# Kernel optimization log

Hardware: AMD Instinct MI355X
Metric: run time of the kernel (lower is better)

## Reference

```python
import jax, jax.numpy as jnp
import numpy as np

EMBED_DIM = 1024
Q_HEADS = 16
KV_HEADS = 8            # n_heads // 2 per CrossAttention
HEAD_DIM = EMBED_DIM // Q_HEADS   # 64
KV_EMBED = HEAD_DIM * KV_HEADS    # 512
GROUPS = Q_HEADS // KV_HEADS      # 2
LN_EPS = 1e-5
RMS_EPS = 1e-6


def _rms_norm(x):
    # SimpleRMSNorm (no learned scale) used inside BitLinear
    return x * jax.lax.rsqrt(jnp.mean(jnp.square(x), axis=-1, keepdims=True) + RMS_EPS)


def _act_quant(x):
    # per-token 8-bit absmax activation quant (BitNet b1.58)
    scale = 127.0 / jnp.maximum(jnp.max(jnp.abs(x), axis=-1, keepdims=True), 1e-5)
    return jnp.clip(jnp.round(x * scale), -128.0, 127.0) / scale


def _weight_quant(w):
    # ternary {-1,0,1} absmean weight quant
    scale = 1.0 / jnp.maximum(jnp.mean(jnp.abs(w)), 1e-5)
    return jnp.clip(jnp.round(w * scale), -1.0, 1.0) / scale


def _ste(a, q):
    # straight-through estimator: forward=q, backward=identity
    return a + jax.lax.stop_gradient(q - a)


def bit_linear(x, w):
    # x: [b, n, in], w: [out, in] (torch Linear layout), no bias
    xn = _rms_norm(x)
    xq = _ste(xn, _act_quant(xn))
    wq = _ste(w, _weight_quant(w))
    return jnp.einsum('bni,oi->bno', xq, wq)


def setup_inputs() -> dict:
    key = jax.random.key(0)
    ks = jax.random.split(key, 6)
    B, N, S, D = 16, 1024, 256, EMBED_DIM
    s = D ** -0.5
    return {
        'x': jax.random.normal(ks[0], (B, N, D), jnp.float32),
        'y': jax.random.normal(ks[1], (B, S, D), jnp.float32),
        'wq': jax.random.normal(ks[2], (D, D), jnp.float32) * s,
        'wk': jax.random.normal(ks[3], (KV_EMBED, D), jnp.float32) * s,
        'wv': jax.random.normal(ks[4], (KV_EMBED, D), jnp.float32) * s,
        'wo': jax.random.normal(ks[5], (D, D), jnp.float32) * s,
        'ln_gamma': jnp.ones((D,), jnp.float32),
        'ln_beta': jnp.zeros((D,), jnp.float32),
    }


def reference(x, y, wq, wk, wv, wo, ln_gamma, ln_beta):
    B, N, D = x.shape
    S = y.shape[1]
    # ternary-quantized projections
    q = bit_linear(x, wq).reshape(B, N, Q_HEADS, HEAD_DIM)
    k = bit_linear(y, wk).reshape(B, S, KV_HEADS, HEAD_DIM)
    v = bit_linear(y, wv).reshape(B, S, KV_HEADS, HEAD_DIM)
    # grouped-query attention: split q heads as (kv_head, group)
    q = jnp.transpose(q, (0, 2, 1, 3)) / (HEAD_DIM ** 0.5)   # [b, Hq, n, d]
    q = q.reshape(B, KV_HEADS, GROUPS, N, HEAD_DIM)           # [b, h, g, n, d]
    k = jnp.transpose(k, (0, 2, 1, 3))                        # [b, h, s, d]
    v = jnp.transpose(v, (0, 2, 1, 3))
    scores = jnp.einsum('bhgnd,bhsd->bhgns', q, k)
    attn = jax.nn.softmax(scores, axis=-1)                    # is_causal=False, no mask
    out = jnp.einsum('bhgns,bhsd->bhgnd', attn, v)
    out = jnp.transpose(out, (0, 3, 1, 2, 4)).reshape(B, N, D)  # b n (h g) d -> b n D
    # LayerNorm before out projection
    mu = jnp.mean(out, axis=-1, keepdims=True)
    var = jnp.mean(jnp.square(out - mu), axis=-1, keepdims=True)
    out = (out - mu) * jax.lax.rsqrt(var + LN_EPS) * ln_gamma + ln_beta
    return bit_linear(out, wo)
```

## Files before the change

kernel.cpp:

```cpp
#include <hip/hip_runtime.h>
#include <hip/hip_bf16.h>

typedef int int4v __attribute__((ext_vector_type(4)));
typedef float float4v __attribute__((ext_vector_type(4)));
typedef _Float16 half8 __attribute__((ext_vector_type(8)));

#define DEV __device__ __forceinline__

DEV signed char quant8(float v) {
    int q = (int)rintf(v);
    q = q < -128 ? -128 : (q > 127 ? 127 : q);
    return (signed char)q;
}

DEV int tern1(float v) {
    int q = (int)rintf(v);
    q = q < -1 ? -1 : (q > 1 ? 1 : q);
    return q;
}

DEV void gl2lds16(const void* g, void* l) {
    __builtin_amdgcn_global_load_lds(
        (const __attribute__((address_space(1))) void*)g,
        (__attribute__((address_space(3))) void*)l, 16, 0, 0);
}

__global__ __launch_bounds__(256) void absmean_all(
    const float* __restrict__ WQ, const float* __restrict__ WK,
    const float* __restrict__ WV, const float* __restrict__ WO,
    double* __restrict__ part)
{
    __shared__ double red[256];
    int bx = blockIdx.x, t = threadIdx.x;
    const float* W; int rel;
    if (bx < 64)       { W = WQ; rel = bx; }
    else if (bx < 96)  { W = WK; rel = bx - 64; }
    else if (bx < 128) { W = WV; rel = bx - 96; }
    else               { W = WO; rel = bx - 128; }
    size_t base = (size_t)rel * 16384;
    double acc = 0.0;
    for (int i = t; i < 16384; i += 256) acc += (double)fabsf(W[base + i]);
    red[t] = acc; __syncthreads();
    #pragma unroll
    for (int o = 128; o > 0; o >>= 1) {
        if (t < o) red[t] += red[t + o];
        __syncthreads();
    }
    if (t == 0) part[bx] = red[0];
}

__global__ __launch_bounds__(256) void betas_kernel(
    const double* __restrict__ part, float* __restrict__ betas)
{
    int t = threadIdx.x, w = t >> 6, lane = t & 63;
    const int offs[4]   = {0, 64, 96, 128};
    const int cnts[4]   = {64, 32, 32, 64};
    const int counts[4] = {1048576, 524288, 524288, 1048576};
    double v = (lane < cnts[w]) ? part[offs[w] + lane] : 0.0;
    #pragma unroll
    for (int o = 32; o > 0; o >>= 1) v += __shfl_down(v, o);
    if (lane == 0) betas[w] = fmaxf((float)(v / (double)counts[w]), 1e-5f);
}

__global__ __launch_bounds__(256) void wquant_all(
    const float* __restrict__ WQ, const float* __restrict__ WK,
    const float* __restrict__ WV, const float* __restrict__ WO,
    signed char* __restrict__ w8, const float* __restrict__ betas)
{
    int bx = blockIdx.x;
    const float* W; signed char* O; float inv; int rel;
    if (bx < 1024)      { W = WQ; O = w8;                           rel = bx;        inv = 1.f / betas[0]; }
    else if (bx < 1536) { W = WK; O = w8 + (1 << 20);               rel = bx - 1024; inv = 1.f / betas[1]; }
    else if (bx < 2048) { W = WV; O = w8 + (1 << 20) + (512 << 10); rel = bx - 1536; inv = 1.f / betas[2]; }
    else                { W = WO; O = w8 + (2 << 20);               rel = bx - 2048; inv = 1.f / betas[3]; }
    int i = rel * 256 + threadIdx.x;
    float4 u = ((const float4*)W)[i];
    int q0 = tern1(u.x * inv);
    int q1 = tern1(u.y * inv);
    int q2 = tern1(u.z * inv);
    int q3 = tern1(u.w * inv);
    int packed = (q0 & 0xff) | ((q1 & 0xff) << 8) | ((q2 & 0xff) << 16) | ((q3 & 0xff) << 24);
    ((int*)O)[i] = packed;
}

__global__ __launch_bounds__(256) void act_quant(
    const float* __restrict__ X, signed char* __restrict__ X8,
    float* __restrict__ RS)
{
    int row = blockIdx.x * 4 + (threadIdx.x >> 6);
    int lane = threadIdx.x & 63;
    const float4* xr = (const float4*)(X + (size_t)row * 1024) + lane * 4;
    float4 u[4];
    #pragma unroll
    for (int i = 0; i < 4; i++) u[i] = xr[i];
    float ss = 0.f, am = 0.f;
    #pragma unroll
    for (int i = 0; i < 4; i++) {
        ss += u[i].x * u[i].x + u[i].y * u[i].y + u[i].z * u[i].z + u[i].w * u[i].w;
        am = fmaxf(am, fmaxf(fmaxf(fabsf(u[i].x), fabsf(u[i].y)),
                             fmaxf(fabsf(u[i].z), fabsf(u[i].w))));
    }
    #pragma unroll
    for (int o = 32; o > 0; o >>= 1) {
        ss += __shfl_xor(ss, o);
        am = fmaxf(am, __shfl_xor(am, o));
    }
    float r = 1.f / sqrtf(ss * (1.f / 1024.f) + 1e-6f);
    float m = fmaxf(am * r, 1e-5f);
    float s = 127.f / m;
    int pk[4];
    #pragma unroll
    for (int i = 0; i < 4; i++) {
        int q0 = quant8((u[i].x * r) * s);
        int q1 = quant8((u[i].y * r) * s);
        int q2 = quant8((u[i].z * r) * s);
        int q3 = quant8((u[i].w * r) * s);
        pk[i] = (q0 & 0xff) | ((q1 & 0xff) << 8) | ((q2 & 0xff) << 16) | ((q3 & 0xff) << 24);
    }
    int4v pv = {pk[0], pk[1], pk[2], pk[3]};
    ((int4v*)(X8 + (size_t)row * 1024))[lane] = pv;
    if (lane == 0) RS[row] = m * (1.f / 127.f);
}

__global__ __launch_bounds__(256) void gemm_i8(
    const signed char* __restrict__ A, const signed char* __restrict__ B,
    float* __restrict__ outF, _Float16* __restrict__ outH,
    _Float16* __restrict__ outK, _Float16* __restrict__ outV,
    int N, int K,
    const float* __restrict__ rowscale, const float* __restrict__ betas,
    int b0i, int b1i, int split, float extra, int mode)
{
    __shared__ __align__(16) signed char As[128 * 64];
    __shared__ __align__(16) signed char Bs[128 * 64];
    const int tid = threadIdx.x;
    const int lane = tid & 63, wid = tid >> 6;
    const int wr = wid >> 1, wc = wid & 1;
    const int lr = lane & 15, quad = lane >> 4;
    const int bM = blockIdx.y, bN = blockIdx.x;

    int4v zero = {0, 0, 0, 0};
    int4v acc[4][4];
    #pragma unroll
    for (int i = 0; i < 4; i++)
        #pragma unroll
        for (int j = 0; j < 4; j++) acc[i][j] = zero;

    const int srow = wid * 32 + (lane >> 2);
    const int soff = (lane & 3) * 16;
    const signed char* gA0 = A + (size_t)(bM * 128 + srow) * K + soff;
    const signed char* gA1 = gA0 + (size_t)16 * K;
    const signed char* gB0 = B + (size_t)(bN * 128 + srow) * K + soff;
    const signed char* gB1 = gB0 + (size_t)16 * K;
    signed char* lA0 = As + wid * 2048;
    signed char* lA1 = lA0 + 1024;
    signed char* lB0 = Bs + wid * 2048;
    signed char* lB1 = lB0 + 1024;

    for (int kb = 0; kb < K; kb += 64) {
        __syncthreads();
        gl2lds16(gA0 + kb, lA0);
        gl2lds16(gA1 + kb, lA1);
        gl2lds16(gB0 + kb, lB0);
        gl2lds16(gB1 + kb, lB1);
        __syncthreads();
        int4v af[4], bfr[4];
        #pragma unroll
        for (int tm = 0; tm < 4; tm++)
            af[tm] = *(const int4v*)(As + (wr * 64 + tm * 16 + lr) * 64 + quad * 16);
        #pragma unroll
        for (int tn = 0; tn < 4; tn++)
            bfr[tn] = *(const int4v*)(Bs + (wc * 64 + tn * 16 + lr) * 64 + quad * 16);
        #pragma unroll
        for (int tm = 0; tm < 4; tm++)
            #pragma unroll
            for (int tn = 0; tn < 4; tn++)
                acc[tm][tn] = __builtin_amdgcn_mfma_i32_16x16x64_i8(af[tm], bfr[tn], acc[tm][tn], 0, 0, 0);
    }

    const float s0 = betas[b0i] * extra, s1 = betas[b1i] * extra;
    #pragma unroll
    for (int tm = 0; tm < 4; tm++) {
        #pragma unroll
        for (int r = 0; r < 4; r++) {
            int grow = bM * 128 + wr * 64 + tm * 16 + quad * 4 + r;
            float rs = rowscale[grow];
            #pragma unroll
            for (int tn = 0; tn < 4; tn++) {
                int col = bN * 128 + wc * 64 + tn * 16 + lr;
                float v = (float)acc[tm][tn][r] * rs * (col < split ? s0 : s1);
                if (mode == 0) {
                    outF[(size_t)grow * N + col] = v;
                } else if (mode == 1) {
                    outH[(size_t)grow * 1024 + col] = (_Float16)v;
                } else {
                    if (col < 512)
                        outK[(size_t)grow * 512 + col] = (_Float16)v;
                    else
                        outV[((size_t)(grow >> 8) * 512 + (col - 512)) * 256 + (grow & 255)] = (_Float16)v;
                }
            }
        }
    }
}

__global__ __launch_bounds__(256, 4) void attn_mfma(
    const _Float16* Qh, const _Float16* __restrict__ Kh,
    const _Float16* __restrict__ Vt, _Float16* Oh)
{
    __shared__ __align__(16) _Float16 KVs[256 * 64];

    const int tid = threadIdx.x;
    const int lane = tid & 63;
    const int w = tid >> 6;
    const int lq = lane & 15;
    const int quad = lane >> 4;
    const int swz = (lq & 7) << 4;

    const int bx = blockIdx.x;
    const int nt = bx & 15, g = (bx >> 4) & 1, h = (bx >> 5) & 7, b = bx >> 8;
    const int rbase = b * 1024 + nt * 64 + w * 16;
    const int qcol0 = (h * 2 + g) * 64;

    half8 aq[2];
    #pragma unroll
    for (int ks = 0; ks < 2; ks++)
        aq[ks] = *(const half8*)(Qh + (size_t)(rbase + lq) * 1024 + qcol0 + ks * 32 + quad * 8);

    {
        int kb = tid >> 3;
        int c  = tid & 7;
        int rp = (kb & 3) | ((kb >> 1) & 12) | ((kb & 4) << 2);
        const _Float16* kg = Kh + (size_t)(b * 256 + kb) * 512 + h * 64 + c * 8;
        char* lb = (char*)KVs;
        #pragma unroll
        for (int j = 0; j < 8; j++) {
            int row = 32 * j + rp;
            int off = (row * 128 + c * 16) ^ ((row & 7) << 4);
            *(half8*)(lb + off) = *(const half8*)(kg + (size_t)32 * j * 512);
        }
    }
    __syncthreads();

    float4v acc[16];
    float4v zf = {0.f, 0.f, 0.f, 0.f};
    #pragma unroll
    for (int t = 0; t < 16; t++) acc[t] = zf;
    const int kc0 = (quad * 16) ^ swz;
    const int kc1 = (64 + quad * 16) ^ swz;
    #pragma unroll
    for (int t = 0; t < 16; t++) {
        const char* krow = (const char*)KVs + (t * 16 + lq) * 128;
        half8 kf0 = *(const half8*)(krow + kc0);
        acc[t] = __builtin_amdgcn_mfma_f32_16x16x32_f16(kf0, aq[0], acc[t], 0, 0, 0);
        half8 kf1 = *(const half8*)(krow + kc1);
        acc[t] = __builtin_amdgcn_mfma_f32_16x16x32_f16(kf1, aq[1], acc[t], 0, 0, 0);
    }

    float m = acc[0][0];
    #pragma unroll
    for (int t = 0; t < 16; t++) {
        #pragma unroll
        for (int r = 0; r < 4; r++) m = fmaxf(m, acc[t][r]);
    }
    m = fmaxf(m, __shfl_xor(m, 16));
    m = fmaxf(m, __shfl_xor(m, 32));
    float l = 0.f;
    #pragma unroll
    for (int t = 0; t < 16; t++) {
        #pragma unroll
        for (int r = 0; r < 4; r++) {
            float p = __expf(acc[t][r] - m);
            acc[t][r] = p;
            l += p;
        }
    }
    l += __shfl_xor(l, 16);
    l += __shfl_xor(l, 32);

    __syncthreads();

    {
        int row = tid >> 5, c = tid & 31;
        const _Float16* vg = Vt + ((size_t)b * 512 + h * 64 + row) * 256 + c * 8;
        char* lb = (char*)KVs;
        #pragma unroll
        for (int j = 0; j < 8; j++) {
            int rr = row + 8 * j;
            int off = (rr * 512 + c * 16) ^ ((rr & 7) << 4);
            *(half8*)(lb + off) = *(const half8*)(vg + (size_t)8 * j * 256);
        }
    }
    __syncthreads();

    float4v oacc[4];
    #pragma unroll
    for (int dt = 0; dt < 4; dt++) oacc[dt] = zf;
    #pragma unroll
    for (int ks = 0; ks < 8; ks++) {
        half8 pf;
        #pragma unroll
        for (int r = 0; r < 4; r++) {
            pf[r]     = (_Float16)acc[2 * ks][r];
            pf[4 + r] = (_Float16)acc[2 * ks + 1][r];
        }
        const int vc = (ks * 64 + quad * 16) ^ swz;
        #pragma unroll
        for (int dt = 0; dt < 4; dt++) {
            half8 bv = *(const half8*)((const char*)KVs + (dt * 16 + lq) * 512 + vc);
            oacc[dt] = __builtin_amdgcn_mfma_f32_16x16x32_f16(pf, bv, oacc[dt], 0, 0, 0);
        }
    }

    float linv = 1.f / l;
    float invr[4];
    #pragma unroll
    for (int r = 0; r < 4; r++) invr[r] = __shfl(linv, quad * 4 + r);
    #pragma unroll
    for (int dt = 0; dt < 4; dt++) {
        #pragma unroll
        for (int r = 0; r < 4; r++) {
            Oh[(size_t)(rbase + quad * 4 + r) * 1024 + qcol0 + dt * 16 + lq] =
                (_Float16)(oacc[dt][r] * invr[r]);
        }
    }
}

__global__ __launch_bounds__(256) void ln_quant(
    const _Float16* __restrict__ AO, const float* __restrict__ G,
    const float* __restrict__ Bt, signed char* __restrict__ O8,
    float* __restrict__ OS)
{
    int row = blockIdx.x * 4 + (threadIdx.x >> 6);
    int lane = threadIdx.x & 63;
    const _Float16* xr = AO + (size_t)row * 1024 + lane * 16;
    half8 h0 = *(const half8*)xr;
    half8 h1 = *(const half8*)(xr + 8);
    float x[16];
    #pragma unroll
    for (int i = 0; i < 8; i++) { x[i] = (float)h0[i]; x[8 + i] = (float)h1[i]; }
    float sx = 0.f, sx2 = 0.f;
    #pragma unroll
    for (int i = 0; i < 16; i++) { sx += x[i]; sx2 += x[i] * x[i]; }
    #pragma unroll
    for (int o = 32; o > 0; o >>= 1) {
        sx += __shfl_xor(sx, o);
        sx2 += __shfl_xor(sx2, o);
    }
    float mu = sx * (1.f / 1024.f);
    float var = sx2 * (1.f / 1024.f) - mu * mu;
    float rstd = 1.f / sqrtf(var + 1e-5f);

    const float4* gp = (const float4*)(G + lane * 16);
    const float4* bp = (const float4*)(Bt + lane * 16);
    float l[16];
    #pragma unroll
    for (int i = 0; i < 4; i++) {
        float4 gv = gp[i], bv = bp[i];
        l[i * 4 + 0] = (x[i * 4 + 0] - mu) * rstd * gv.x + bv.x;
        l[i * 4 + 1] = (x[i * 4 + 1] - mu) * rstd * gv.y + bv.y;
        l[i * 4 + 2] = (x[i * 4 + 2] - mu) * rstd * gv.z + bv.z;
        l[i * 4 + 3] = (x[i * 4 + 3] - mu) * rstd * gv.w + bv.w;
    }
    float msq = 0.f, am = 0.f;
    #pragma unroll
    for (int i = 0; i < 16; i++) { msq += l[i] * l[i]; am = fmaxf(am, fabsf(l[i])); }
    #pragma unroll
    for (int o = 32; o > 0; o >>= 1) {
        msq += __shfl_xor(msq, o);
        am = fmaxf(am, __shfl_xor(am, o));
    }
    float r2 = 1.f / sqrtf(msq * (1.f / 1024.f) + 1e-6f);
    float mx = fmaxf(am * r2, 1e-5f);
    float s = 127.f / mx;
    int pk[4];
    #pragma unroll
    for (int i = 0; i < 4; i++) {
        int q0 = quant8((l[i * 4 + 0] * r2) * s);
        int q1 = quant8((l[i * 4 + 1] * r2) * s);
        int q2 = quant8((l[i * 4 + 2] * r2) * s);
        int q3 = quant8((l[i * 4 + 3] * r2) * s);
        pk[i] = (q0 & 0xff) | ((q1 & 0xff) << 8) | ((q2 & 0xff) << 16) | ((q3 & 0xff) << 24);
    }
    int4v pv = {pk[0], pk[1], pk[2], pk[3]};
    ((int4v*)(O8 + (size_t)row * 1024))[lane] = pv;
    if (lane == 0) OS[row] = mx * (1.f / 127.f);
}

extern "C" void kernel_launch(void* const* d_in, const int* in_sizes, int n_in,
                              void* d_out, int out_size, void* d_ws, size_t ws_size,
                              hipStream_t stream)
{
    const float* X  = (const float*)d_in[0];
    const float* Y  = (const float*)d_in[1];
    const float* WQ = (const float*)d_in[2];
    const float* WK = (const float*)d_in[3];
    const float* WV = (const float*)d_in[4];
    const float* WO = (const float*)d_in[5];
    const float* G  = (const float*)d_in[6];
    const float* Bt = (const float*)d_in[7];

    char* ws = (char*)d_ws;
    float*  betas = (float*)ws;
    double* part  = (double*)(ws + 256);
    char* w8  = ws + 4096;
    char* x8  = w8 + (3 << 20);
    char* y8  = x8 + (16 << 20);
    float* xs = (float*)(y8 + (4 << 20));
    float* ys = xs + 16384;
    float* os = ys + 4096;
    _Float16* qf16 = (_Float16*)(os + 16384);
    _Float16* kf16 = qf16 + (size_t)16384 * 1024;
    _Float16* vt16 = kf16 + (size_t)4096 * 512;
    char* wq8 = w8;
    char* kv8 = w8 + (1 << 20);
    char* wo8 = w8 + (2 << 20);
    char* o8  = x8;

    absmean_all<<<192, 256, 0, stream>>>(WQ, WK, WV, WO, part);
    betas_kernel<<<1, 256, 0, stream>>>(part, betas);
    wquant_all<<<3072, 256, 0, stream>>>(WQ, WK, WV, WO, (signed char*)w8, betas);

    act_quant<<<4096, 256, 0, stream>>>(X, (signed char*)x8, xs);
    act_quant<<<1024, 256, 0, stream>>>(Y, (signed char*)y8, ys);

    gemm_i8<<<dim3(8, 128), 256, 0, stream>>>(
        (signed char*)x8, (signed char*)wq8, nullptr, qf16, nullptr, nullptr,
        1024, 1024, xs, betas, 0, 0, 1024, 0.125f, 1);
    gemm_i8<<<dim3(8, 32), 256, 0, stream>>>(
        (signed char*)y8, (signed char*)kv8, nullptr, nullptr, kf16, vt16,
        1024, 1024, ys, betas, 1, 2, 512, 1.f, 2);

    attn_mfma<<<4096, 256, 0, stream>>>(qf16, kf16, vt16, qf16);

    ln_quant<<<4096, 256, 0, stream>>>(qf16, G, Bt, (signed char*)o8, os);

    gemm_i8<<<dim3(8, 128), 256, 0, stream>>>(
        (signed char*)o8, (signed char*)wo8, (float*)d_out, nullptr, nullptr, nullptr,
        1024, 1024, os, betas, 3, 3, 1024, 1.f, 0);
}
```

Before: 350.1 us.

## Double-buffer LDS tiles in int8 GEMM and remap blocks across XCDs

The int8 MFMA GEMM now keeps two LDS buffers for the A and B tiles. It issues the global-to-LDS loads for the next 64-wide K slice before computing on the current one, so load latency overlaps with MFMA work and each K step needs one barrier instead of two. Block indices are also remapped so consecutive hardware block IDs, which are spread round-robin over XCDs, handle nearby output tiles and can share cache. The cost is double the LDS per block, which may lower occupancy. The code assumes K is a multiple of 128, the grid is 8 blocks wide, and the block count divides by 8.

```diff
diff --git a/kernel.cpp b/kernel.cpp
--- a/kernel.cpp
+++ b/kernel.cpp
@@ -130,13 +130,19 @@
     const float* __restrict__ rowscale, const float* __restrict__ betas,
     int b0i, int b1i, int split, float extra, int mode)
 {
-    __shared__ __align__(16) signed char As[128 * 64];
-    __shared__ __align__(16) signed char Bs[128 * 64];
+    __shared__ __align__(16) signed char As0[128 * 64];
+    __shared__ __align__(16) signed char Bs0[128 * 64];
+    __shared__ __align__(16) signed char As1[128 * 64];
+    __shared__ __align__(16) signed char Bs1[128 * 64];
     const int tid = threadIdx.x;
     const int lane = tid & 63, wid = tid >> 6;
     const int wr = wid >> 1, wc = wid & 1;
     const int lr = lane & 15, quad = lane >> 4;
-    const int bM = blockIdx.y, bN = blockIdx.x;
+
+    const int flat = blockIdx.y * 8 + blockIdx.x;
+    const int chunk = (gridDim.x * gridDim.y) >> 3;
+    const int f2 = (flat & 7) * chunk + (flat >> 3);
+    const int bM = f2 >> 3, bN = f2 & 7;
 
     int4v zero = {0, 0, 0, 0};
     int4v acc[4][4];
@@ -151,31 +157,49 @@
     const signed char* gA1 = gA0 + (size_t)16 * K;
     const signed char* gB0 = B + (size_t)(bN * 128 + srow) * K + soff;
     const signed char* gB1 = gB0 + (size_t)16 * K;
-    signed char* lA0 = As + wid * 2048;
-    signed char* lA1 = lA0 + 1024;
-    signed char* lB0 = Bs + wid * 2048;
-    signed char* lB1 = lB0 + 1024;
-
-    for (int kb = 0; kb < K; kb += 64) {
+    const int lo0 = wid * 2048, lo1 = wid * 2048 + 1024;
+
+    gl2lds16(gA0, As0 + lo0);
+    gl2lds16(gA1, As0 + lo1);
+    gl2lds16(gB0, Bs0 + lo0);
+    gl2lds16(gB1, Bs0 + lo1);
+    __syncthreads();
+
+#define GEMM_COMPUTE(AS, BS)                                                   \
+    {                                                                          \
+        int4v af[4], bfr[4];                                                   \
+        _Pragma("unroll")                                                      \
+        for (int tm = 0; tm < 4; tm++)                                         \
+            af[tm] = *(const int4v*)((AS) + (wr * 64 + tm * 16 + lr) * 64 + quad * 16); \
+        _Pragma("unroll")                                                      \
+        for (int tn = 0; tn < 4; tn++)                                         \
+            bfr[tn] = *(const int4v*)((BS) + (wc * 64 + tn * 16 + lr) * 64 + quad * 16); \
+        _Pragma("unroll")                                                      \
+        for (int tm = 0; tm < 4; tm++)                                         \
+            _Pragma("unroll")                                                  \
+            for (int tn = 0; tn < 4; tn++)                                     \
+                acc[tm][tn] = __builtin_amdgcn_mfma_i32_16x16x64_i8(af[tm], bfr[tn], acc[tm][tn], 0, 0, 0); \
+    }
+
+    for (int kb = 0; kb < K; kb += 128) {
+        if (kb + 64 < K) {
+            gl2lds16(gA0 + kb + 64, As1 + lo0);
+            gl2lds16(gA1 + kb + 64, As1 + lo1);
+            gl2lds16(gB0 + kb + 64, Bs1 + lo0);
+            gl2lds16(gB1 + kb + 64, Bs1 + lo1);
+        }
+        GEMM_COMPUTE(As0, Bs0);
         __syncthreads();
-        gl2lds16(gA0 + kb, lA0);
-        gl2lds16(gA1 + kb, lA1);
-        gl2lds16(gB0 + kb, lB0);
-        gl2lds16(gB1 + kb, lB1);
+        if (kb + 128 < K) {
+            gl2lds16(gA0 + kb + 128, As0 + lo0);
+            gl2lds16(gA1 + kb + 128, As0 + lo1);
+            gl2lds16(gB0 + kb + 128, Bs0 + lo0);
+            gl2lds16(gB1 + kb + 128, Bs0 + lo1);
+        }
+        GEMM_COMPUTE(As1, Bs1);
         __syncthreads();
-        int4v af[4], bfr[4];
-        #pragma unroll
-        for (int tm = 0; tm < 4; tm++)
-            af[tm] = *(const int4v*)(As + (wr * 64 + tm * 16 + lr) * 64 + quad * 16);
-        #pragma unroll
-        for (int tn = 0; tn < 4; tn++)
-            bfr[tn] = *(const int4v*)(Bs + (wc * 64 + tn * 16 + lr) * 64 + quad * 16);
-        #pragma unroll
-        for (int tm = 0; tm < 4; tm++)
-            #pragma unroll
-            for (int tn = 0; tn < 4; tn++)
-                acc[tm][tn] = __builtin_amdgcn_mfma_i32_16x16x64_i8(af[tm], bfr[tn], acc[tm][tn], 0, 0, 0);
-    }
+    }
+#undef GEMM_COMPUTE
 
     const float s0 = betas[b0i] * extra, s1 = betas[b1i] * extra;
     #pragma unroll
```

Result: faster. 324.2 us (-7.4%).

## Triple-buffer int8 GEMM LDS loads and remap blocks across XCDs

Applied to the files above, without the earlier changes.

Replaces the single-buffered K loop of the int8 GEMM with a three-stage LDS ring. It prefetches two tiles ahead and uses explicit vmcnt waits with a single barrier per iteration, so global-to-LDS loads overlap the MFMA work. It also remaps the block index so that consecutive blocks are spread across the eight XCDs in contiguous chunks. The loop count is now hardcoded to K=1024 and the grid width to 8 column blocks, which makes the kernel wrong for any other shape. Tripling the LDS footprint may also lower occupancy.

```diff
diff --git a/kernel.cpp b/kernel.cpp
--- a/kernel.cpp
+++ b/kernel.cpp
@@ -130,13 +130,17 @@
     const float* __restrict__ rowscale, const float* __restrict__ betas,
     int b0i, int b1i, int split, float extra, int mode)
 {
-    __shared__ __align__(16) signed char As[128 * 64];
-    __shared__ __align__(16) signed char Bs[128 * 64];
+    __shared__ __align__(16) signed char As[3][128 * 64];
+    __shared__ __align__(16) signed char Bs[3][128 * 64];
     const int tid = threadIdx.x;
     const int lane = tid & 63, wid = tid >> 6;
     const int wr = wid >> 1, wc = wid & 1;
     const int lr = lane & 15, quad = lane >> 4;
-    const int bM = blockIdx.y, bN = blockIdx.x;
+
+    const int flat = blockIdx.y * 8 + blockIdx.x;
+    const int chunk = (gridDim.x * gridDim.y) >> 3;
+    const int f2 = (flat & 7) * chunk + (flat >> 3);
+    const int bM = f2 >> 3, bN = f2 & 7;
 
     int4v zero = {0, 0, 0, 0};
     int4v acc[4][4];
@@ -151,31 +155,41 @@
     const signed char* gA1 = gA0 + (size_t)16 * K;
     const signed char* gB0 = B + (size_t)(bN * 128 + srow) * K + soff;
     const signed char* gB1 = gB0 + (size_t)16 * K;
-    signed char* lA0 = As + wid * 2048;
-    signed char* lA1 = lA0 + 1024;
-    signed char* lB0 = Bs + wid * 2048;
-    signed char* lB1 = lB0 + 1024;
-
-    for (int kb = 0; kb < K; kb += 64) {
-        __syncthreads();
-        gl2lds16(gA0 + kb, lA0);
-        gl2lds16(gA1 + kb, lA1);
-        gl2lds16(gB0 + kb, lB0);
-        gl2lds16(gB1 + kb, lB1);
-        __syncthreads();
+    const int lo0 = wid * 2048, lo1 = wid * 2048 + 1024;
+
+#define STAGE(bi, kb)                          \
+    do {                                       \
+        gl2lds16(gA0 + (kb), As[bi] + lo0);    \
+        gl2lds16(gA1 + (kb), As[bi] + lo1);    \
+        gl2lds16(gB0 + (kb), Bs[bi] + lo0);    \
+        gl2lds16(gB1 + (kb), Bs[bi] + lo1);    \
+    } while (0)
+
+    STAGE(0, 0);
+    STAGE(1, 64);
+
+    #pragma unroll
+    for (int t = 0; t < 16; ++t) {
+        if (t < 15) asm volatile("s_waitcnt vmcnt(4)" ::: "memory");
+        else        asm volatile("s_waitcnt vmcnt(0)" ::: "memory");
+        __builtin_amdgcn_s_barrier();
+        if (t + 2 < 16) STAGE((t + 2) % 3, (t + 2) * 64);
+        const signed char* AS = As[t % 3];
+        const signed char* BS = Bs[t % 3];
         int4v af[4], bfr[4];
         #pragma unroll
         for (int tm = 0; tm < 4; tm++)
-            af[tm] = *(const int4v*)(As + (wr * 64 + tm * 16 + lr) * 64 + quad * 16);
+            af[tm] = *(const int4v*)(AS + (wr * 64 + tm * 16 + lr) * 64 + quad * 16);
         #pragma unroll
         for (int tn = 0; tn < 4; tn++)
-            bfr[tn] = *(const int4v*)(Bs + (wc * 64 + tn * 16 + lr) * 64 + quad * 16);
+            bfr[tn] = *(const int4v*)(BS + (wc * 64 + tn * 16 + lr) * 64 + quad * 16);
         #pragma unroll
         for (int tm = 0; tm < 4; tm++)
             #pragma unroll
             for (int tn = 0; tn < 4; tn++)
                 acc[tm][tn] = __builtin_amdgcn_mfma_i32_16x16x64_i8(af[tm], bfr[tn], acc[tm][tn], 0, 0, 0);
     }
+#undef STAGE
 
     const float s0 = betas[b0i] * extra, s1 = betas[b1i] * extra;
     #pragma unroll
```

Result: faster. 322.1 us (-8.0%).
